# Kernel optimization log

Measured on AMD Instinct MI355X. Metric: run time of the kernel, lower is better.

## Reference

```python
import jax, jax.numpy as jnp
import numpy as np

N_NODES = 100000
N_EDGES = 1600000
N_GRAPHS = 128
IN_FEATS = 128
OUT_FEATS = 64


def setup_inputs() -> dict:
    key = jax.random.key(0)
    k1, k2, k3, k4, k5, k6 = jax.random.split(key, 6)
    features = jax.random.normal(k1, (N_NODES, IN_FEATS), jnp.float32)
    src = jax.random.randint(k2, (N_EDGES,), 0, N_NODES, dtype=jnp.int32)
    dst = jax.random.randint(k3, (N_EDGES,), 0, N_NODES, dtype=jnp.int32)
    graph_ids = jnp.sort(jax.random.randint(k4, (N_NODES,), 0, N_GRAPHS, dtype=jnp.int32))
    # Xavier-uniform init as in DGL GraphConv
    lim1 = float(np.sqrt(6.0 / (IN_FEATS + IN_FEATS)))
    lim2 = float(np.sqrt(6.0 / (IN_FEATS + OUT_FEATS)))
    W1 = jax.random.uniform(k5, (IN_FEATS, IN_FEATS), jnp.float32, -lim1, lim1)
    W2 = jax.random.uniform(k6, (IN_FEATS, OUT_FEATS), jnp.float32, -lim2, lim2)
    b1 = jnp.zeros((IN_FEATS,), jnp.float32)
    b2 = jnp.zeros((OUT_FEATS,), jnp.float32)
    return {"features": features, "W1": W1, "b1": b1, "W2": W2, "b2": b2,
            "src": src, "dst": dst, "graph_ids": graph_ids, "num_graphs": N_GRAPHS}


def _graph_conv(x, W, b, src, dst, n_nodes):
    # DGL GraphConv, norm='both': D_dst^{-1/2} A D_src^{-1/2} X W + b
    ones = jnp.ones(src.shape, x.dtype)
    deg_out = jax.ops.segment_sum(ones, src, num_segments=n_nodes)
    deg_in = jax.ops.segment_sum(ones, dst, num_segments=n_nodes)
    norm_src = jax.lax.rsqrt(jnp.maximum(deg_out, 1.0))  # [N]
    norm_dst = jax.lax.rsqrt(jnp.maximum(deg_in, 1.0))   # [N]
    h = (x * norm_src[:, None]) @ W                       # dense transform first
    agg = jax.ops.segment_sum(h[src], dst, num_segments=n_nodes)  # spmm-style scatter-add
    return agg * norm_dst[:, None] + b


def reference(features, W1, b1, W2, b2, src, dst, graph_ids, num_graphs):
    n = features.shape[0]
    h = jax.nn.relu(_graph_conv(features, W1, b1, src, dst, n))
    h = jax.nn.relu(_graph_conv(h, W2, b2, src, dst, n))
    # dgl.mean_nodes: per-graph mean over nodes
    sums = jax.ops.segment_sum(h, graph_ids, num_segments=num_graphs)
    counts = jax.ops.segment_sum(jnp.ones((n, 1), h.dtype), graph_ids, num_segments=num_graphs)
    return sums / jnp.maximum(counts, 1.0)
```

## Files before the change

### kernel.cpp

```cpp
#include <hip/hip_runtime.h>
#include <hip/hip_bf16.h>


#define NPP_SHIFT 9
#define NPP 512
#define MAXP 256
#define NB 512
#define CAPB 1280

typedef __attribute__((ext_vector_type(8))) short frag8;
typedef __attribute__((ext_vector_type(4))) float f32x4;
typedef __attribute__((ext_vector_type(2))) float v2f;

__launch_bounds__(256)
__global__ void buildAC(const int* __restrict__ src, const int* __restrict__ dst,
                        int E, int P, int* __restrict__ cur,
                        int* __restrict__ ebuf_src, int2* __restrict__ ebuf_dst,
                        const int* __restrict__ gids, int N, int G,
                        int* __restrict__ gcnt) {
    __shared__ int hs[MAXP], hd[MAXP], bs1[MAXP], bs2[MAXP], hg[MAXP];
    int tid = threadIdx.x;
    int stripe = blockIdx.x & 7;
    for (int i = tid; i < MAXP; i += 256) { hs[i] = 0; hd[i] = 0; hg[i] = 0; }
    __syncthreads();
    int per_block = (E + NB - 1) / NB;
    int e0 = blockIdx.x * per_block;
    int e1 = min(e0 + per_block, E);
    for (int e = e0 + tid; e < e1; e += 256) {
        atomicAdd(&hs[src[e] >> NPP_SHIFT], 1);
        atomicAdd(&hd[dst[e] >> NPP_SHIFT], 1);
    }
    int npb = (N + NB - 1) / NB;
    int n0 = blockIdx.x * npb;
    int n1 = min(n0 + npb, N);
    for (int i = n0 + tid; i < n1; i += 256) atomicAdd(&hg[gids[i]], 1);
    __syncthreads();
    for (int p = tid; p < P; p += 256) {
        int c1 = hs[p];
        bs1[p] = c1 ? atomicAdd(&cur[(p << 3) | stripe], c1) : 0;
        int c2 = hd[p];
        bs2[p] = c2 ? atomicAdd(&cur[P * 8 + ((p << 3) | stripe)], c2) : 0;
        hs[p] = 0;
        hd[p] = 0;
    }
    for (int i = tid; i < G; i += 256)
        if (hg[i]) atomicAdd(&gcnt[i], hg[i]);
    __syncthreads();
    for (int e = e0 + tid; e < e1; e += 256) {
        int s = src[e];
        int d = dst[e];
        int p1 = s >> NPP_SHIFT;
        int p2 = d >> NPP_SHIFT;
        int l1 = atomicAdd(&hs[p1], 1);
        ebuf_src[(size_t)((p1 << 3) | stripe) * CAPB + bs1[p1] + l1] = s;
        int l2 = atomicAdd(&hd[p2], 1);
        ebuf_dst[(size_t)((p2 << 3) | stripe) * CAPB + bs2[p2] + l2] = make_int2(d, s);
    }
}

__launch_bounds__(512)
__global__ void passD3(const int* __restrict__ ebuf_src, const int2* __restrict__ ebuf_dst,
                       const int* __restrict__ cur, float* __restrict__ norm_src,
                       int* __restrict__ row_start, int* __restrict__ csr_src,
                       int N, int E, int P) {
    __shared__ int hs[NPP], hd[NPP], sc[NPP];
    int tid = threadIdx.x;
    int p = blockIdx.x;
    int tot = 0;
    if (tid < P) {
#pragma unroll
        for (int t = 0; t < 8; ++t) tot += cur[P * 8 + (tid << 3) + t];
    }
    sc[tid] = tot;
    __syncthreads();
    for (int off = 1; off < 512; off <<= 1) {
        int t = (tid >= off) ? sc[tid - off] : 0;
        __syncthreads();
        sc[tid] += t;
        __syncthreads();
    }
    int gbase = (p > 0) ? sc[p - 1] : 0;
    __syncthreads();
    int node_lo = p << NPP_SHIFT;
    int nl = min(NPP, N - node_lo);
    hs[tid] = 0;
    hd[tid] = 0;
    __syncthreads();
#pragma unroll
    for (int t = 0; t < 8; ++t) {
        int cnt = cur[(p << 3) + t];
        const int* eb = ebuf_src + (size_t)((p << 3) + t) * CAPB;
        for (int i = tid; i < cnt; i += 512)
            atomicAdd(&hs[eb[i] - node_lo], 1);
    }
#pragma unroll
    for (int t = 0; t < 8; ++t) {
        int cnt = cur[P * 8 + (p << 3) + t];
        const int2* eb = ebuf_dst + (size_t)((p << 3) + t) * CAPB;
        for (int i = tid; i < cnt; i += 512)
            atomicAdd(&hd[eb[i].x - node_lo], 1);
    }
    __syncthreads();
    if (tid < nl) norm_src[node_lo + tid] = rsqrtf((float)max(hs[tid], 1));
    int myh = hd[tid];
    sc[tid] = myh;
    __syncthreads();
    for (int off = 1; off < 512; off <<= 1) {
        int t = (tid >= off) ? sc[tid - off] : 0;
        __syncthreads();
        sc[tid] += t;
        __syncthreads();
    }
    int row0 = gbase + sc[tid] - myh;
    if (tid < nl) row_start[node_lo + tid] = row0;
    if (p == P - 1 && tid == 0) row_start[N] = E;
    __syncthreads();
    hd[tid] = row0;
    __syncthreads();
#pragma unroll
    for (int t = 0; t < 8; ++t) {
        int cnt = cur[P * 8 + (p << 3) + t];
        const int2* eb = ebuf_dst + (size_t)((p << 3) + t) * CAPB;
        for (int i = tid; i < cnt; i += 512) {
            int2 r = eb[i];
            int pos = atomicAdd(&hd[r.x - node_lo], 1);
            csr_src[pos] = r.y;
        }
    }
}

template <int COLS, bool BF16IN, bool PERM, bool FP8OUT>
__launch_bounds__(256)
__global__ void gemm_mfma(const void* __restrict__ xin, const float* __restrict__ w,
                          const float* __restrict__ norm,
                          void* __restrict__ out, int n) {
    constexpr int NT = COLS / 16;
    __shared__ short wlds[4 * NT * 64 * 8];
    const int tid = threadIdx.x;
    for (int i = tid; i < 128 * COLS / 4; i += 256) {
        int k = (i * 4) / COLS;
        int n0 = (i * 4) % COLS;
        float4 wv;
        if constexpr (PERM) {
            int ksrc = 64 * ((k >> 2) & 1) + 16 * (k & 3) + (k >> 3);
            wv = *reinterpret_cast<const float4*>(w + (size_t)ksrc * COLS + n0);
        } else {
            wv = reinterpret_cast<const float4*>(w)[i];
        }
        int c = k >> 5, q = (k >> 3) & 3, j = k & 7;
        float vals[4] = {wv.x, wv.y, wv.z, wv.w};
#pragma unroll
        for (int u = 0; u < 4; ++u) {
            int nn = n0 + u;
            int t = nn >> 4;
            int ln = (q << 4) | (nn & 15);
            union { __hip_bfloat16 b; short s; } cv;
            cv.b = __float2bfloat16(vals[u]);
            wlds[(((c * NT + t) << 6) | ln) * 8 + j] = cv.s;
        }
    }
    __syncthreads();

    const int lane = tid & 63;
    const int wid = tid >> 6;
    const int m = lane & 15;
    const int q = lane >> 4;
    const int ntiles = (n + 15) >> 4;
    const frag8* wfr = reinterpret_cast<const frag8*>(wlds);

    for (int wt = blockIdx.x * 4 + wid; wt < ntiles; wt += gridDim.x * 4) {
        const int row = (wt << 4) + m;
        frag8 af[4];
        if (row < n) {
            if constexpr (BF16IN) {
                const frag8* xp = reinterpret_cast<const frag8*>(
                    (const __hip_bfloat16*)xin + (size_t)row * 128);
#pragma unroll
                for (int c = 0; c < 4; ++c) af[c] = xp[c * 4 + q];
            } else {
                const float* xp = (const float*)xin + (size_t)row * 128;
                float nm = norm[row];
#pragma unroll
                for (int c = 0; c < 4; ++c) {
                    int base = c * 32 + q * 8;
                    float4 v0 = *reinterpret_cast<const float4*>(xp + base);
                    float4 v1 = *reinterpret_cast<const float4*>(xp + base + 4);
                    union { frag8 f; short s[8]; } a;
                    union { __hip_bfloat16 b; short s; } cv;
                    cv.b = __float2bfloat16(v0.x * nm); a.s[0] = cv.s;
                    cv.b = __float2bfloat16(v0.y * nm); a.s[1] = cv.s;
                    cv.b = __float2bfloat16(v0.z * nm); a.s[2] = cv.s;
                    cv.b = __float2bfloat16(v0.w * nm); a.s[3] = cv.s;
                    cv.b = __float2bfloat16(v1.x * nm); a.s[4] = cv.s;
                    cv.b = __float2bfloat16(v1.y * nm); a.s[5] = cv.s;
                    cv.b = __float2bfloat16(v1.z * nm); a.s[6] = cv.s;
                    cv.b = __float2bfloat16(v1.w * nm); a.s[7] = cv.s;
                    af[c] = a.f;
                }
            }
        } else {
#pragma unroll
            for (int c = 0; c < 4; ++c) af[c] = frag8{0, 0, 0, 0, 0, 0, 0, 0};
        }
        f32x4 acc[NT] = {};
#pragma unroll
        for (int c = 0; c < 4; ++c)
#pragma unroll
            for (int t = 0; t < NT; ++t)
                acc[t] = __builtin_amdgcn_mfma_f32_16x16x32_bf16(
                    af[c], wfr[(c * NT + t) * 64 + lane], acc[t], 0, 0, 0);
#pragma unroll
        for (int r = 0; r < 4; ++r) {
            int grow = (wt << 4) + q * 4 + r;
            if (grow < n) {
                if constexpr (FP8OUT && COLS == 128) {
                    uint w0 = 0, w1 = 0;
                    w0 = (uint)__builtin_amdgcn_cvt_pk_fp8_f32(acc[0][r], acc[1][r], (int)w0, false);
                    w0 = (uint)__builtin_amdgcn_cvt_pk_fp8_f32(acc[2][r], acc[3][r], (int)w0, true);
                    w1 = (uint)__builtin_amdgcn_cvt_pk_fp8_f32(acc[4][r], acc[5][r], (int)w1, false);
                    w1 = (uint)__builtin_amdgcn_cvt_pk_fp8_f32(acc[6][r], acc[7][r], (int)w1, true);
                    reinterpret_cast<uint2*>(out)[(size_t)grow * 16 + m] = make_uint2(w0, w1);
                } else if constexpr (FP8OUT) {
                    uint w0 = 0;
                    w0 = (uint)__builtin_amdgcn_cvt_pk_fp8_f32(acc[0][r], acc[1][r], (int)w0, false);
                    w0 = (uint)__builtin_amdgcn_cvt_pk_fp8_f32(acc[2][r], acc[3][r], (int)w0, true);
                    reinterpret_cast<uint*>(out)[(size_t)grow * 16 + m] = w0;
                } else {
                    __hip_bfloat16* ob = reinterpret_cast<__hip_bfloat16*>(out);
#pragma unroll
                    for (int t = 0; t < NT; ++t)
                        ob[(size_t)grow * COLS + t * 16 + m] = __float2bfloat16(acc[t][r]);
                }
            }
        }
    }
}

__launch_bounds__(256)
__global__ void spmm1_kernel(const uint2* __restrict__ h1,
                             const int* __restrict__ row_start,
                             const int* __restrict__ csr_src,
                             const float* __restrict__ b1,
                             const float* __restrict__ norm_src,
                             uint4* __restrict__ x2n, int n) {
    int wv = (blockIdx.x * blockDim.x + threadIdx.x) >> 6;
    int lane = threadIdx.x & 63;
    int r0 = wv * 2;
    if (r0 >= n) return;
    int a = lane >> 4;
    int s = lane & 15;
    int e0[2], e1[2];
#pragma unroll
    for (int r = 0; r < 2; ++r) {
        int rr = min(r0 + r, n - 1);
        e0[r] = row_start[rr];
        e1[r] = row_start[rr + 1];
        if (r0 + r >= n) e1[r] = e0[r];
    }
    v2f acc[2][4] = {};
    int nb = max((e1[0] - e0[0] + 15) >> 4, (e1[1] - e0[1] + 15) >> 4);
    for (int b = 0; b < nb; ++b) {
        uint2 v[2][4];
#pragma unroll
        for (int r = 0; r < 2; ++r) {
            int base = e0[r] + b * 16;
            if (base + 16 <= e1[r]) {
#pragma unroll
                for (int j = 0; j < 4; ++j)
                    v[r][j] = h1[(size_t)csr_src[base + 4 * j + a] * 16 + s];
            } else if (base < e1[r]) {
#pragma unroll
                for (int j = 0; j < 4; ++j) {
                    int idx = base + 4 * j + a;
                    int cidx = min(idx, e1[r] - 1);
                    uint2 vv = h1[(size_t)csr_src[cidx] * 16 + s];
                    bool ok = idx < e1[r];
                    v[r][j].x = ok ? vv.x : 0u;
                    v[r][j].y = ok ? vv.y : 0u;
                }
            } else {
#pragma unroll
                for (int j = 0; j < 4; ++j) v[r][j] = make_uint2(0u, 0u);
            }
        }
#pragma unroll
        for (int r = 0; r < 2; ++r)
#pragma unroll
            for (int j = 0; j < 4; ++j) {
                acc[r][0] += __builtin_amdgcn_cvt_pk_f32_fp8((int)v[r][j].x, false);
                acc[r][1] += __builtin_amdgcn_cvt_pk_f32_fp8((int)v[r][j].x, true);
                acc[r][2] += __builtin_amdgcn_cvt_pk_f32_fp8((int)v[r][j].y, false);
                acc[r][3] += __builtin_amdgcn_cvt_pk_f32_fp8((int)v[r][j].y, true);
            }
    }
#pragma unroll
    for (int r = 0; r < 2; ++r)
#pragma unroll
        for (int k = 0; k < 4; ++k) {
            v2f t;
            t[0] = __shfl_xor(acc[r][k][0], 16);
            t[1] = __shfl_xor(acc[r][k][1], 16);
            acc[r][k] += t;
            t[0] = __shfl_xor(acc[r][k][0], 32);
            t[1] = __shfl_xor(acc[r][k][1], 32);
            acc[r][k] += t;
        }
    if (a == 0) {
        float bbl[4] = {b1[s], b1[32 + s], b1[64 + s], b1[96 + s]};
        float bbh[4] = {b1[16 + s], b1[48 + s], b1[80 + s], b1[112 + s]};
#pragma unroll
        for (int r = 0; r < 2; ++r) {
            if (r0 + r < n) {
                float nd = rsqrtf((float)max(e1[r] - e0[r], 1));
                float ns = norm_src[r0 + r];
                uint w[4];
#pragma unroll
                for (int k = 0; k < 4; ++k) {
                    float fl = fmaxf(fmaf(acc[r][k][0], nd, bbl[k]), 0.f) * ns;
                    float fh = fmaxf(fmaf(acc[r][k][1], nd, bbh[k]), 0.f) * ns;
                    union { __hip_bfloat16 b; ushort u; } cl, ch;
                    cl.b = __float2bfloat16(fl);
                    ch.b = __float2bfloat16(fh);
                    w[k] = (uint)cl.u | ((uint)ch.u << 16);
                }
                x2n[(size_t)(r0 + r) * 16 + s] = make_uint4(w[0], w[1], w[2], w[3]);
            }
        }
    }
}

__launch_bounds__(256)
__global__ void spmm2_kernel(const uint* __restrict__ h2,
                             const int* __restrict__ row_start,
                             const int* __restrict__ csr_src,
                             const float* __restrict__ b2,
                             const int* __restrict__ gids,
                             const int* __restrict__ gcnt,
                             float* __restrict__ out, int n) {
    int wv = (blockIdx.x * blockDim.x + threadIdx.x) >> 6;
    int lane = threadIdx.x & 63;
    int wave = threadIdx.x >> 6;
    int r0 = wv * 4;
    int a = lane >> 4;
    int s = lane & 15;
    int e0[4], e1[4], g[4];
    float inv[4];
#pragma unroll
    for (int r = 0; r < 4; ++r) {
        int rr = min(r0 + r, n - 1);
        e0[r] = row_start[rr];
        e1[r] = row_start[rr + 1];
        g[r] = gids[rr];
        if (r0 + r >= n) { e1[r] = e0[r]; g[r] = -1; }
        inv[r] = 1.f / (float)max(gcnt[max(g[r], 0)], 1);
    }
    float acc[4][4] = {};
    int nb = 0;
#pragma unroll
    for (int r = 0; r < 4; ++r) nb = max(nb, (e1[r] - e0[r] + 15) >> 4);
    for (int b = 0; b < nb; ++b) {
        uint u[4][4];
#pragma unroll
        for (int r = 0; r < 4; ++r) {
            int base = e0[r] + b * 16;
            if (base + 16 <= e1[r]) {
#pragma unroll
                for (int j = 0; j < 4; ++j)
                    u[r][j] = h2[(size_t)csr_src[base + 4 * j + a] * 16 + s];
            } else if (base < e1[r]) {
#pragma unroll
                for (int j = 0; j < 4; ++j) {
                    int idx = base + 4 * j + a;
                    int cidx = min(idx, e1[r] - 1);
                    uint vv = h2[(size_t)csr_src[cidx] * 16 + s];
                    u[r][j] = (idx < e1[r]) ? vv : 0u;
                }
            } else {
#pragma unroll
                for (int j = 0; j < 4; ++j) u[r][j] = 0u;
            }
        }
#pragma unroll
        for (int r = 0; r < 4; ++r)
#pragma unroll
            for (int j = 0; j < 4; ++j) {
                v2f lo = __builtin_amdgcn_cvt_pk_f32_fp8((int)u[r][j], false);
                v2f hi = __builtin_amdgcn_cvt_pk_f32_fp8((int)u[r][j], true);
                acc[r][0] += lo[0]; acc[r][1] += lo[1];
                acc[r][2] += hi[0]; acc[r][3] += hi[1];
            }
    }
#pragma unroll
    for (int r = 0; r < 4; ++r)
#pragma unroll
        for (int k = 0; k < 4; ++k) {
            acc[r][k] += __shfl_xor(acc[r][k], 16);
            acc[r][k] += __shfl_xor(acc[r][k], 32);
        }
    float bb0 = b2[s], bb1 = b2[16 + s], bb2v = b2[32 + s], bb3 = b2[48 + s];
    float val[4][4];
#pragma unroll
    for (int r = 0; r < 4; ++r) {
        float nd = rsqrtf((float)max(e1[r] - e0[r], 1));
        bool vld = g[r] >= 0;
        val[r][0] = vld ? fmaxf(fmaf(acc[r][0], nd, bb0), 0.f) * inv[r] : 0.f;
        val[r][1] = vld ? fmaxf(fmaf(acc[r][1], nd, bb1), 0.f) * inv[r] : 0.f;
        val[r][2] = vld ? fmaxf(fmaf(acc[r][2], nd, bb2v), 0.f) * inv[r] : 0.f;
        val[r][3] = vld ? fmaxf(fmaf(acc[r][3], nd, bb3), 0.f) * inv[r] : 0.f;
    }
    __shared__ float sbuf[4][64];
    __shared__ int sg[4];
    bool same = (g[0] == g[1]) && (g[1] == g[2]) && (g[2] == g[3]) && (g[0] >= 0);
    int sgw;
    if (same) {
        if (a == 0) {
            sbuf[wave][s]      = val[0][0] + val[1][0] + val[2][0] + val[3][0];
            sbuf[wave][16 + s] = val[0][1] + val[1][1] + val[2][1] + val[3][1];
            sbuf[wave][32 + s] = val[0][2] + val[1][2] + val[2][2] + val[3][2];
            sbuf[wave][48 + s] = val[0][3] + val[1][3] + val[2][3] + val[3][3];
        }
        sgw = g[0];
    } else {
        if (a == 0) {
#pragma unroll
            for (int r = 0; r < 4; ++r) {
                if (g[r] >= 0) {
                    atomicAdd(&out[(size_t)g[r] * 64 + s], val[r][0]);
                    atomicAdd(&out[(size_t)g[r] * 64 + 16 + s], val[r][1]);
                    atomicAdd(&out[(size_t)g[r] * 64 + 32 + s], val[r][2]);
                    atomicAdd(&out[(size_t)g[r] * 64 + 48 + s], val[r][3]);
                }
            }
            sbuf[wave][s] = 0.f;
            sbuf[wave][16 + s] = 0.f;
            sbuf[wave][32 + s] = 0.f;
            sbuf[wave][48 + s] = 0.f;
        }
        sgw = -1;
    }
    if (lane == 0) sg[wave] = sgw;
    __syncthreads();
    if (wave == 0) {
        int g0 = sg[0], g1 = sg[1], g2 = sg[2], g3 = sg[3];
        if (g0 == g1 && g1 == g2 && g2 == g3 && g0 >= 0) {
            float ssum = sbuf[0][lane] + sbuf[1][lane] + sbuf[2][lane] + sbuf[3][lane];
            atomicAdd(&out[(size_t)g0 * 64 + lane], ssum);
        } else {
#pragma unroll
            for (int w = 0; w < 4; ++w)
                if (sg[w] >= 0)
                    atomicAdd(&out[(size_t)sg[w] * 64 + lane], sbuf[w][lane]);
        }
    }
}

extern "C" void kernel_launch(void* const* d_in, const int* in_sizes, int n_in,
                              void* d_out, int out_size, void* d_ws, size_t ws_size,
                              hipStream_t stream) {
    const float* features = (const float*)d_in[0];
    const float* W1 = (const float*)d_in[1];
    const float* b1 = (const float*)d_in[2];
    const float* W2 = (const float*)d_in[3];
    const float* b2 = (const float*)d_in[4];
    const int* src = (const int*)d_in[5];
    const int* dst = (const int*)d_in[6];
    const int* gids = (const int*)d_in[7];
    const int N = in_sizes[7];
    const int E = in_sizes[5];
    const int G = out_size / 64;
    float* out = (float*)d_out;
    const int P = (N + NPP - 1) >> NPP_SHIFT;

    char* ws = (char*)d_ws;
    size_t off = 0;
    auto alloc = [&](size_t bytes) -> void* {
        void* p = ws + off;
        off = (off + bytes + 255) & ~(size_t)255;
        return p;
    };
    int* zblock = (int*)alloc((size_t)(G + 16 * P) * 4);
    int* gcnt = zblock;
    int* cur = zblock + G;
    int* ebuf_src = (int*)alloc((size_t)P * 8 * CAPB * 4);
    int2* ebuf_dst = (int2*)alloc((size_t)P * 8 * CAPB * 8);
    float* norm_src = (float*)alloc((size_t)N * 4);
    int* row_start = (int*)alloc((size_t)(N + 1) * 4);
    int* csr_src = (int*)alloc((size_t)E * 4);
    uint* h1 = (uint*)alloc((size_t)N * 128);
    __hip_bfloat16* x2n = (__hip_bfloat16*)alloc((size_t)N * 128 * 2);
    uint* h2 = h1;

    hipMemsetAsync(out, 0, (size_t)out_size * sizeof(float), stream);
    hipMemsetAsync(zblock, 0, (size_t)(G + 16 * P) * 4, stream);

    buildAC<<<NB, 256, 0, stream>>>(src, dst, E, P, cur, ebuf_src, ebuf_dst,
                                    gids, N, G, gcnt);
    passD3<<<P, 512, 0, stream>>>(ebuf_src, ebuf_dst, cur, norm_src, row_start,
                                  csr_src, N, E, P);

    gemm_mfma<128, false, false, true><<<768, 256, 0, stream>>>(features, W1, norm_src,
                                                                (void*)h1, N);
    {
        int waves = (N + 1) / 2;
        int blocks = (waves * 64 + 255) / 256;
        spmm1_kernel<<<blocks, 256, 0, stream>>>((const uint2*)h1, row_start, csr_src, b1,
                                                 norm_src, (uint4*)x2n, N);
    }
    gemm_mfma<64, true, true, true><<<768, 256, 0, stream>>>(x2n, W2, nullptr,
                                                             (void*)h2, N);
    {
        int waves = (N + 3) / 4;
        int blocks = (waves * 64 + 255) / 256;
        spmm2_kernel<<<blocks, 256, 0, stream>>>(h2, row_start, csr_src, b2,
                                                 gids, gcnt, out, N);
    }
}
```

Before: 285.1 us.

## Halve CSR-build partitions, pack edge buffers, and stage dst edges in LDS

Partitions shrink from 512 to 256 nodes, which doubles the number of blocks in the CSR build pass. Edge buffers are now compressed: src-degree entries become a single byte holding the local node index, and dst entries become one uint packing the 8-bit local dst with the 17-bit src. The second pass loads each partition's dst edges into LDS once and reuses them for both the histogram and the scatter, rather than reading global memory twice. This cuts global traffic in the preprocessing kernels, but it relies on N fitting in 17 bits and on per-partition edge counts fitting under the LDS and bucket capacities.

```diff
diff --git a/kernel.cpp b/kernel.cpp
--- a/kernel.cpp
+++ b/kernel.cpp
@@ -2,11 +2,12 @@
 #include <hip/hip_bf16.h>
 
 
-#define NPP_SHIFT 9
-#define NPP 512
-#define MAXP 256
+#define NPP_SHIFT 8
+#define NPP 256
+#define MAXP 512
 #define NB 512
-#define CAPB 1280
+#define CAPB 704
+#define EBMAX 4608
 
 typedef __attribute__((ext_vector_type(8))) short frag8;
 typedef __attribute__((ext_vector_type(4))) float f32x4;
@@ -15,13 +16,14 @@
 __launch_bounds__(256)
 __global__ void buildAC(const int* __restrict__ src, const int* __restrict__ dst,
                         int E, int P, int* __restrict__ cur,
-                        int* __restrict__ ebuf_src, int2* __restrict__ ebuf_dst,
+                        unsigned char* __restrict__ ebuf_src, uint* __restrict__ ebuf_dst,
                         const int* __restrict__ gids, int N, int G,
                         int* __restrict__ gcnt) {
-    __shared__ int hs[MAXP], hd[MAXP], bs1[MAXP], bs2[MAXP], hg[MAXP];
+    __shared__ int hs[MAXP], hd[MAXP], bs1[MAXP], bs2[MAXP], hg[256];
     int tid = threadIdx.x;
     int stripe = blockIdx.x & 7;
-    for (int i = tid; i < MAXP; i += 256) { hs[i] = 0; hd[i] = 0; hg[i] = 0; }
+    for (int i = tid; i < MAXP; i += 256) { hs[i] = 0; hd[i] = 0; }
+    for (int i = tid; i < 256; i += 256) hg[i] = 0;
     __syncthreads();
     int per_block = (E + NB - 1) / NB;
     int e0 = blockIdx.x * per_block;
@@ -52,26 +54,39 @@
         int p1 = s >> NPP_SHIFT;
         int p2 = d >> NPP_SHIFT;
         int l1 = atomicAdd(&hs[p1], 1);
-        ebuf_src[(size_t)((p1 << 3) | stripe) * CAPB + bs1[p1] + l1] = s;
+        ebuf_src[(size_t)((p1 << 3) | stripe) * CAPB + bs1[p1] + l1] =
+            (unsigned char)(s & 255);
         int l2 = atomicAdd(&hd[p2], 1);
-        ebuf_dst[(size_t)((p2 << 3) | stripe) * CAPB + bs2[p2] + l2] = make_int2(d, s);
+        ebuf_dst[(size_t)((p2 << 3) | stripe) * CAPB + bs2[p2] + l2] =
+            ((uint)(d & 255) << 17) | (uint)s;
     }
 }
 
 __launch_bounds__(512)
-__global__ void passD3(const int* __restrict__ ebuf_src, const int2* __restrict__ ebuf_dst,
+__global__ void passD5(const unsigned char* __restrict__ ebuf_src,
+                       const uint* __restrict__ ebuf_dst,
                        const int* __restrict__ cur, float* __restrict__ norm_src,
                        int* __restrict__ row_start, int* __restrict__ csr_src,
                        int N, int E, int P) {
-    __shared__ int hs[NPP], hd[NPP], sc[NPP];
+    __shared__ uint eb[EBMAX];
+    __shared__ int hs[NPP], hd[NPP], sc[512], to[9];
     int tid = threadIdx.x;
     int p = blockIdx.x;
+    if (tid == 0) {
+        int run = 0;
+        for (int t = 0; t < 8; ++t) {
+            to[t] = run;
+            run += cur[P * 8 + (p << 3) + t];
+        }
+        to[8] = run;
+    }
     int tot = 0;
     if (tid < P) {
 #pragma unroll
         for (int t = 0; t < 8; ++t) tot += cur[P * 8 + (tid << 3) + t];
     }
     sc[tid] = tot;
+    if (tid < NPP) { hs[tid] = 0; hd[tid] = 0; }
     __syncthreads();
     for (int off = 1; off < 512; off <<= 1) {
         int t = (tid >= off) ? sc[tid - off] : 0;
@@ -80,29 +95,26 @@
         __syncthreads();
     }
     int gbase = (p > 0) ? sc[p - 1] : 0;
+#pragma unroll
+    for (int t = 0; t < 8; ++t) {
+        int cnt = to[t + 1] - to[t];
+        const uint* ebg = ebuf_dst + (size_t)((p << 3) + t) * CAPB;
+        for (int i = tid; i < cnt; i += 512) eb[to[t] + i] = ebg[i];
+    }
+    __syncthreads();
+    int total = to[8];
+    for (int i = tid; i < total; i += 512) atomicAdd(&hd[eb[i] >> 17], 1);
+#pragma unroll
+    for (int t = 0; t < 8; ++t) {
+        int cnt = cur[(p << 3) + t];
+        const unsigned char* ebg = ebuf_src + (size_t)((p << 3) + t) * CAPB;
+        for (int i = tid; i < cnt; i += 512) atomicAdd(&hs[ebg[i]], 1);
+    }
     __syncthreads();
     int node_lo = p << NPP_SHIFT;
     int nl = min(NPP, N - node_lo);
-    hs[tid] = 0;
-    hd[tid] = 0;
-    __syncthreads();
-#pragma unroll
-    for (int t = 0; t < 8; ++t) {
-        int cnt = cur[(p << 3) + t];
-        const int* eb = ebuf_src + (size_t)((p << 3) + t) * CAPB;
-        for (int i = tid; i < cnt; i += 512)
-            atomicAdd(&hs[eb[i] - node_lo], 1);
-    }
-#pragma unroll
-    for (int t = 0; t < 8; ++t) {
-        int cnt = cur[P * 8 + (p << 3) + t];
-        const int2* eb = ebuf_dst + (size_t)((p << 3) + t) * CAPB;
-        for (int i = tid; i < cnt; i += 512)
-            atomicAdd(&hd[eb[i].x - node_lo], 1);
-    }
-    __syncthreads();
     if (tid < nl) norm_src[node_lo + tid] = rsqrtf((float)max(hs[tid], 1));
-    int myh = hd[tid];
+    int myh = (tid < NPP) ? hd[tid] : 0;
     sc[tid] = myh;
     __syncthreads();
     for (int off = 1; off < 512; off <<= 1) {
@@ -111,21 +123,17 @@
         sc[tid] += t;
         __syncthreads();
     }
-    int row0 = gbase + sc[tid] - myh;
-    if (tid < nl) row_start[node_lo + tid] = row0;
+    if (tid < NPP) {
+        int row0 = gbase + sc[tid] - myh;
+        if (tid < nl) row_start[node_lo + tid] = row0;
+        hd[tid] = row0;
+    }
     if (p == P - 1 && tid == 0) row_start[N] = E;
     __syncthreads();
-    hd[tid] = row0;
-    __syncthreads();
-#pragma unroll
-    for (int t = 0; t < 8; ++t) {
-        int cnt = cur[P * 8 + (p << 3) + t];
-        const int2* eb = ebuf_dst + (size_t)((p << 3) + t) * CAPB;
-        for (int i = tid; i < cnt; i += 512) {
-            int2 r = eb[i];
-            int pos = atomicAdd(&hd[r.x - node_lo], 1);
-            csr_src[pos] = r.y;
-        }
+    for (int i = tid; i < total; i += 512) {
+        uint r = eb[i];
+        int pos = atomicAdd(&hd[r >> 17], 1);
+        csr_src[pos] = (int)(r & 0x1FFFFu);
     }
 }
 
@@ -481,8 +489,8 @@
     int* zblock = (int*)alloc((size_t)(G + 16 * P) * 4);
     int* gcnt = zblock;
     int* cur = zblock + G;
-    int* ebuf_src = (int*)alloc((size_t)P * 8 * CAPB * 4);
-    int2* ebuf_dst = (int2*)alloc((size_t)P * 8 * CAPB * 8);
+    unsigned char* ebuf_src = (unsigned char*)alloc((size_t)P * 8 * CAPB);
+    uint* ebuf_dst = (uint*)alloc((size_t)P * 8 * CAPB * 4);
     float* norm_src = (float*)alloc((size_t)N * 4);
     int* row_start = (int*)alloc((size_t)(N + 1) * 4);
     int* csr_src = (int*)alloc((size_t)E * 4);
@@ -495,7 +503,7 @@
 
     buildAC<<<NB, 256, 0, stream>>>(src, dst, E, P, cur, ebuf_src, ebuf_dst,
                                     gids, N, G, gcnt);
-    passD3<<<P, 512, 0, stream>>>(ebuf_src, ebuf_dst, cur, norm_src, row_start,
+    passD5<<<P, 512, 0, stream>>>(ebuf_src, ebuf_dst, cur, norm_src, row_start,
                                   csr_src, N, E, P);
 
     gemm_mfma<128, false, false, true><<<768, 256, 0, stream>>>(features, W1, norm_src,
```

Measured after the change: 285.3 us. No clear change (+0.1%).
